# Optimization experiments

Measured on AMD Instinct MI355X. Metric: run time of the kernel, lower is better.

The kernel has to match this reference:

```python
import jax, jax.numpy as jnp
from jax import lax
import numpy as np

B, S, H = 8, 512, 768


def setup_inputs() -> dict:
    key = jax.random.key(0)
    ks = jax.random.split(key, 8)
    outputs = jax.random.normal(ks[0], (B, S, H), dtype=jnp.float32)
    starts = jax.random.randint(ks[1], (B,), S // 4, 3 * S // 4)
    mask = jnp.stack([starts, jnp.full((B,), S, dtype=starts.dtype)], axis=1)  # [B,2]
    sc = 1.0 / np.sqrt(H)
    Wa_w = jax.random.normal(ks[2], (H, H), dtype=jnp.float32) * sc
    Wa_b = jax.random.normal(ks[3], (H,), dtype=jnp.float32) * sc
    Ua_w = jax.random.normal(ks[4], (H, H), dtype=jnp.float32) * sc
    Ua_b = jax.random.normal(ks[5], (H,), dtype=jnp.float32) * sc
    Va_w = jax.random.normal(ks[6], (1, H), dtype=jnp.float32) * sc
    Va_b = jax.random.normal(ks[7], (1,), dtype=jnp.float32) * sc
    return {"outputs": outputs, "mask": mask, "Wa_w": Wa_w, "Wa_b": Wa_b,
            "Ua_w": Ua_w, "Ua_b": Ua_b, "Va_w": Va_w, "Va_b": Va_b}


def reference(outputs, mask, Wa_w, Wa_b, Ua_w, Ua_b, Va_w, Va_b):
    # outputs: [B,S,H]; mask[:,0] = start (source = tokens [0:start], summary = [start:S])
    b, s, h = outputs.shape
    Wq = jnp.einsum('bsh,oh->bso', outputs, Wa_w) + Wa_b  # query proj, [B,S,H]
    Uk = jnp.einsum('bsh,oh->bso', outputs, Ua_w) + Ua_b  # key proj,   [B,S,H]
    va = Va_w[0]  # [H]
    vb = Va_b[0]

    # Stream over query token positions to avoid a [B,S,S,H] tanh intermediate.
    def step(_, wq_t):  # wq_t: [B,H]
        m = jnp.tanh(wq_t[:, None, :] + Uk)          # [B,S,H]
        sc_t = jnp.einsum('bkh,h->bk', m, va) + vb   # [B,S]
        return None, sc_t

    _, scores = lax.scan(step, None, jnp.swapaxes(Wq, 0, 1))  # [S(query token), B, S(key)]
    scores = jnp.swapaxes(scores, 0, 1)  # [B, S_token, S_key]

    start = mask[:, 0]                              # [B]
    j = jnp.arange(s)
    # summary query j corresponds to token index start + j
    t_idx = jnp.clip(start[:, None] + j[None, :], 0, s - 1)            # [B,S]
    sc = jnp.take_along_axis(scores, t_idx[:, :, None], axis=1)       # [B,S,S]
    key_mask = (j[None, :] < start[:, None])                           # [B,S] valid source keys
    q_mask = (j[None, :] < (s - start)[:, None])                       # [B,S] valid summary queries

    sc = jnp.where(key_mask[:, None, :], sc, -1e30)
    w = jax.nn.softmax(sc, axis=-1)
    # zero out exactly where the torch code leaves zeros
    attentions = w * key_mask[:, None, :].astype(w.dtype) * q_mask[:, :, None].astype(w.dtype)
    contexts = jnp.einsum('bjk,bkh->bjh', attentions, outputs)
    return attentions, contexts
```

## Files before the change

kernel.cpp:

```cpp
#include <hip/hip_runtime.h>

typedef float  f32x4   __attribute__((ext_vector_type(4)));
typedef short  short8  __attribute__((ext_vector_type(8)));
typedef unsigned short ushort8 __attribute__((ext_vector_type(8)));

constexpr int kB = 8;
constexpr int kS = 512;
constexpr int kH = 768;
constexpr int kJM = 384;

constexpr float kTanhScale = 2.8853900817779268f;

__device__ __forceinline__ float native_exp2(float x) {
    float r; asm("v_exp_f32 %0, %1" : "=v"(r) : "v"(x)); return r;
}

__device__ __forceinline__ float waveMax(float v) {
#pragma unroll
    for (int off = 32; off > 0; off >>= 1) v = fmaxf(v, __shfl_xor(v, off, 64));
    return v;
}
__device__ __forceinline__ float waveSum(float v) {
#pragma unroll
    for (int off = 32; off > 0; off >>= 1) v += __shfl_xor(v, off, 64);
    return v;
}

__global__ __launch_bounds__(256) void k0_convert(
    const float* __restrict__ X, const float* __restrict__ Wa, const float* __restrict__ Ua,
    unsigned short* __restrict__ Xhi, unsigned short* __restrict__ Xlo,
    unsigned short* __restrict__ Wahi, unsigned short* __restrict__ Walo,
    unsigned short* __restrict__ Uahi, unsigned short* __restrict__ Ualo)
{
    const int i4 = blockIdx.x * 256 + threadIdx.x;
    const float* src; unsigned short *hi, *lo; int off;
    if (i4 < 786432)      { src = X;  hi = Xhi;  lo = Xlo;  off = i4; }
    else if (i4 < 933888) { src = Wa; hi = Wahi; lo = Walo; off = i4 - 786432; }
    else                  { src = Ua; hi = Uahi; lo = Ualo; off = i4 - 933888; }

    float4 v = *(const float4*)(src + (size_t)off * 4);
    unsigned short h[4], l[4];
#pragma unroll
    for (int c = 0; c < 4; ++c) {
        float x = (&v.x)[c];
        unsigned u = __float_as_uint(x);
        h[c] = (unsigned short)(u >> 16);
        float hf = __uint_as_float(u & 0xFFFF0000u);
        l[c] = (unsigned short)(__float_as_uint(x - hf) >> 16);
    }
    *(ushort4*)(hi + (size_t)off * 4) = make_ushort4(h[0], h[1], h[2], h[3]);
    *(ushort4*)(lo + (size_t)off * 4) = make_ushort4(l[0], l[1], l[2], l[3]);
}

__global__ __launch_bounds__(256) void k1_mfma(
    const unsigned short* __restrict__ Xhi, const unsigned short* __restrict__ Xlo,
    const unsigned short* __restrict__ W0hi, const unsigned short* __restrict__ W0lo,
    const unsigned short* __restrict__ W1hi, const unsigned short* __restrict__ W1lo,
    const float* __restrict__ b0, const float* __restrict__ b1,
    const int* __restrict__ mask,
    float* __restrict__ Eqc, float* __restrict__ EkTc)
{
    __shared__ char smem[49664];
    unsigned short* Ahi = (unsigned short*)smem;
    unsigned short* Alo = (unsigned short*)(smem + 10240);
    unsigned short* Bhi = (unsigned short*)(smem + 20480);
    unsigned short* Blo = (unsigned short*)(smem + 28160);

    const int z = blockIdx.z;
    const unsigned short* Whi = z ? W1hi : W0hi;
    const unsigned short* Wlo = z ? W1lo : W0lo;
    const float* bias = z ? b1 : b0;

    const int m0 = blockIdx.y * 128;
    const int n0 = blockIdx.x * 96;
    const int t  = threadIdx.x;
    const int bI = m0 >> 9;
    const int lb = m0 & (kS - 1);
    const int start = mask[2 * bI];

    if (z == 0) { if (lb + 128 <= start) return; }
    else        { if (lb >= start) return; }

    const int ar = t >> 1, ko = (t & 1) << 4;
    const bool doB = (ar < 96);
    const size_t aoff = (size_t)(m0 + ar) * kH + ko;
    const size_t woff = (size_t)(n0 + ar) * kH + ko;

    const int wid = t >> 6, lane = t & 63;
    const int wr = wid >> 1, wc = wid & 1;
    const int lr = lane & 15, lk = (lane >> 4) << 3;

    f32x4 acc[4][3];
#pragma unroll
    for (int mi = 0; mi < 4; ++mi)
#pragma unroll
        for (int ni = 0; ni < 3; ++ni)
#pragma unroll
            for (int r = 0; r < 4; ++r) acc[mi][ni][r] = 0.0f;

    for (int h0 = 0; h0 < kH; h0 += 32) {
        ushort8 ah0 = *(const ushort8*)(Xhi + aoff + h0);
        ushort8 ah1 = *(const ushort8*)(Xhi + aoff + h0 + 8);
        ushort8 al0 = *(const ushort8*)(Xlo + aoff + h0);
        ushort8 al1 = *(const ushort8*)(Xlo + aoff + h0 + 8);
        ushort8 bh0, bh1, bl0, bl1;
        if (doB) {
            bh0 = *(const ushort8*)(Whi + woff + h0);
            bh1 = *(const ushort8*)(Whi + woff + h0 + 8);
            bl0 = *(const ushort8*)(Wlo + woff + h0);
            bl1 = *(const ushort8*)(Wlo + woff + h0 + 8);
        }
        __syncthreads();
        *(ushort8*)(Ahi + ar * 40 + ko)     = ah0;
        *(ushort8*)(Ahi + ar * 40 + ko + 8) = ah1;
        *(ushort8*)(Alo + ar * 40 + ko)     = al0;
        *(ushort8*)(Alo + ar * 40 + ko + 8) = al1;
        if (doB) {
            *(ushort8*)(Bhi + ar * 40 + ko)     = bh0;
            *(ushort8*)(Bhi + ar * 40 + ko + 8) = bh1;
            *(ushort8*)(Blo + ar * 40 + ko)     = bl0;
            *(ushort8*)(Blo + ar * 40 + ko + 8) = bl1;
        }
        __syncthreads();

        short8 ah[4], al_[4], bh[3], bl[3];
#pragma unroll
        for (int mi = 0; mi < 4; ++mi) {
            const int row = wr * 64 + mi * 16 + lr;
            ah[mi]  = *(const short8*)(Ahi + row * 40 + lk);
            al_[mi] = *(const short8*)(Alo + row * 40 + lk);
        }
#pragma unroll
        for (int ni = 0; ni < 3; ++ni) {
            const int row = wc * 48 + ni * 16 + lr;
            bh[ni] = *(const short8*)(Bhi + row * 40 + lk);
            bl[ni] = *(const short8*)(Blo + row * 40 + lk);
        }
#pragma unroll
        for (int mi = 0; mi < 4; ++mi)
#pragma unroll
            for (int ni = 0; ni < 3; ++ni)
                acc[mi][ni] = __builtin_amdgcn_mfma_f32_16x16x32_bf16(ah[mi], bh[ni], acc[mi][ni], 0, 0, 0);
#pragma unroll
        for (int mi = 0; mi < 4; ++mi)
#pragma unroll
            for (int ni = 0; ni < 3; ++ni)
                acc[mi][ni] = __builtin_amdgcn_mfma_f32_16x16x32_bf16(al_[mi], bh[ni], acc[mi][ni], 0, 0, 0);
#pragma unroll
        for (int mi = 0; mi < 4; ++mi)
#pragma unroll
            for (int ni = 0; ni < 3; ++ni)
                acc[mi][ni] = __builtin_amdgcn_mfma_f32_16x16x32_bf16(ah[mi], bl[ni], acc[mi][ni], 0, 0, 0);
    }

    if (z == 0) {
#pragma unroll
        for (int mi = 0; mi < 4; ++mi)
#pragma unroll
            for (int ni = 0; ni < 3; ++ni) {
                const int ml = lb + wr * 64 + mi * 16 + ((lane >> 4) << 2);
                const int ng = n0 + wc * 48 + ni * 16 + lr;
                const float bn = bias[ng];
#pragma unroll
                for (int r = 0; r < 4; ++r) {
                    const int jj = ml + r - start;
                    if (jj >= 0)
                        Eqc[((size_t)bI * kJM + jj) * kH + ng] =
                            native_exp2((acc[mi][ni][r] + bn) * kTanhScale);
                }
            }
    } else {
        __syncthreads();
        float* stg = (float*)smem;
#pragma unroll
        for (int mi = 0; mi < 4; ++mi)
#pragma unroll
            for (int ni = 0; ni < 3; ++ni) {
                const int ml = wr * 64 + mi * 16 + ((lane >> 4) << 2);
                const int nl = wc * 48 + ni * 16 + lr;
                const float bn = bias[n0 + nl];
#pragma unroll
                for (int r = 0; r < 4; ++r)
                    stg[(ml + r) * 97 + nl] = native_exp2((acc[mi][ni][r] + bn) * kTanhScale);
            }
        __syncthreads();
        const int s4 = (t & 31) << 2, hb_ = t >> 5;
        const int sg = lb + s4;
#pragma unroll
        for (int u = 0; u < 12; ++u) {
            const int h = (u << 3) + hb_;
            float o[4] = { stg[(s4 + 0) * 97 + h], stg[(s4 + 1) * 97 + h],
                           stg[(s4 + 2) * 97 + h], stg[(s4 + 3) * 97 + h] };
            float* dst = EkTc + ((size_t)bI * kH + n0 + h) * kJM + sg;
            if (sg + 3 < start) {
                *(float4*)dst = make_float4(o[0], o[1], o[2], o[3]);
            } else {
#pragma unroll
                for (int e2 = 0; e2 < 4; ++e2)
                    if (sg + e2 < start) dst[e2] = o[e2];
            }
        }
    }
}

__global__ void k2a_worklist(const int* __restrict__ mask, int* __restrict__ wl)
{
    __shared__ int ne[kB], off[kB];
    const int tid = threadIdx.x;
    if (tid < kB) {
        int start = mask[2 * tid];
        ne[tid] = ((kS - start + 1) >> 1) * ((start + 63) >> 6) * 2;
    }
    __syncthreads();
    if (tid == 0) {
        int s = 0;
        for (int b = 0; b < kB; ++b) { off[b] = s; s += ne[b]; }
        wl[0] = s;
    }
    __syncthreads();
    for (int b = 0; b < kB; ++b) {
        int start = mask[2 * b];
        int nkw = (start + 63) >> 6;
        int n = ne[b], base = off[b];
        for (int t = tid; t < n; t += blockDim.x) {
            int c = t & 1, p = t >> 1;
            int jt = p / nkw, kt = p - jt * nkw;
            wl[1 + base + t] = (b << 16) | (jt << 8) | (kt << 1) | c;
        }
    }
}

__global__ __launch_bounds__(256) void k2_scores(
    const float* __restrict__ Eqc, const float* __restrict__ EkTc,
    const float* __restrict__ va, const int* __restrict__ mask,
    const int* __restrict__ wl, float* __restrict__ part0, float* __restrict__ part1)
{
    const int ntiles = wl[0];
    const int lane = threadIdx.x & 63;
    const int wslot = (blockIdx.x << 2) | (threadIdx.x >> 6);
    const int nslots = gridDim.x << 2;

    for (int w = wslot; w < ntiles; w += nslots) {
        const int e = __builtin_amdgcn_readfirstlane(wl[1 + w]);
        const int b = e >> 16, jt = (e >> 8) & 255, ktc = e & 255;
        const int kt = ktc >> 1, c = ktc & 1;
        const int start = __builtin_amdgcn_readfirstlane(mask[2 * b]);
        const int jmax = kS - start;
        const int j0 = jt << 1, k0 = kt << 6;
        const int hbase = c * 384;

        const float* eq0 = Eqc + ((size_t)b * kJM + j0) * kH + hbase;
        const float* eq1 = eq0 + kH;
        const float* ekp = EkTc + ((size_t)b * kH + hbase) * kJM + k0 + lane;
        const float* vap = va + hbase;

        float a0 = 0.0f, a1 = 0.0f;
        float eA[8], eB[8];
#pragma unroll
        for (int c2 = 0; c2 < 8; ++c2) eA[c2] = ekp[(size_t)c2 * kJM];
#pragma unroll
        for (int c2 = 0; c2 < 8; ++c2) eB[c2] = ekp[(size_t)(8 + c2) * kJM];

        for (int h0 = 0; h0 < 384; h0 += 16) {
            const bool more = (h0 + 16) < 384;
            float nA[8], nB[8];
            if (more) {
#pragma unroll
                for (int c2 = 0; c2 < 8; ++c2) nA[c2] = ekp[(size_t)(h0 + 16 + c2) * kJM];
            }
#pragma unroll
            for (int c2 = 0; c2 < 8; ++c2) {
                const float vc = vap[h0 + c2];
                float r0 = __builtin_amdgcn_rcpf(fmaf(eq0[h0 + c2], eA[c2], 1.0f));
                float r1 = __builtin_amdgcn_rcpf(fmaf(eq1[h0 + c2], eA[c2], 1.0f));
                a0 = fmaf(vc, r0, a0);
                a1 = fmaf(vc, r1, a1);
            }
            if (more) {
#pragma unroll
                for (int c2 = 0; c2 < 8; ++c2) nB[c2] = ekp[(size_t)(h0 + 24 + c2) * kJM];
#pragma unroll
                for (int c2 = 0; c2 < 8; ++c2) {
                    const float vc = vap[h0 + 8 + c2];
                    float r0 = __builtin_amdgcn_rcpf(fmaf(eq0[h0 + 8 + c2], eB[c2], 1.0f));
                    float r1 = __builtin_amdgcn_rcpf(fmaf(eq1[h0 + 8 + c2], eB[c2], 1.0f));
                    a0 = fmaf(vc, r0, a0);
                    a1 = fmaf(vc, r1, a1);
                }
#pragma unroll
                for (int c2 = 0; c2 < 8; ++c2) { eA[c2] = nA[c2]; eB[c2] = nB[c2]; }
            } else {
#pragma unroll
                for (int c2 = 0; c2 < 8; ++c2) {
                    const float vc = vap[h0 + 8 + c2];
                    float r0 = __builtin_amdgcn_rcpf(fmaf(eq0[h0 + 8 + c2], eB[c2], 1.0f));
                    float r1 = __builtin_amdgcn_rcpf(fmaf(eq1[h0 + 8 + c2], eB[c2], 1.0f));
                    a0 = fmaf(vc, r0, a0);
                    a1 = fmaf(vc, r1, a1);
                }
            }
        }

        float* srow = (c ? part1 : part0) + ((size_t)b * kS + j0) * kS + k0 + lane;
        if (j0 < jmax)     srow[0]  = -2.0f * a0;
        if (j0 + 1 < jmax) srow[kS] = -2.0f * a1;
    }
}

__global__ __launch_bounds__(256) void k3_softmax(
    float* __restrict__ attn, const float* __restrict__ part1,
    const int* __restrict__ mask)
{
    const int bx = blockIdx.x;
    const int b = bx >> 9;
    const int j = bx & (kS - 1);
    const int start = mask[2 * b];
    float* row = attn + ((size_t)b * kS + j) * kS;
    const int tid = threadIdx.x;

    if (j >= kS - start) {
        row[tid] = 0.0f;
        row[tid + 256] = 0.0f;
        return;
    }

    const float* p1row = part1 + ((size_t)b * kS + j) * kS;
    float v0 = (tid < start) ? row[tid] + p1row[tid] : -1e30f;
    float v1 = (tid + 256 < start) ? row[tid + 256] + p1row[tid + 256] : -1e30f;

    __shared__ float red[4];
    const int wid = tid >> 6;

    float m = waveMax(fmaxf(v0, v1));
    if ((tid & 63) == 0) red[wid] = m;
    __syncthreads();
    m = fmaxf(fmaxf(red[0], red[1]), fmaxf(red[2], red[3]));
    __syncthreads();

    float e0 = (tid < start) ? __expf(v0 - m) : 0.0f;
    float e1 = (tid + 256 < start) ? __expf(v1 - m) : 0.0f;
    float s = waveSum(e0 + e1);
    if ((tid & 63) == 0) red[wid] = s;
    __syncthreads();
    s = red[0] + red[1] + red[2] + red[3];

    float inv = __builtin_amdgcn_rcpf(s);
    row[tid] = e0 * inv;
    row[tid + 256] = e1 * inv;
}

__global__ __launch_bounds__(256) void k4_context(
    const float* __restrict__ attn, const float* __restrict__ outs,
    const int* __restrict__ mask, float* __restrict__ ctx)
{
    const int b = blockIdx.z;
    const int start = mask[2 * b];
    const int kmax = (start + 15) & ~15;
    const int m0 = blockIdx.y * 64;
    const int n0 = blockIdx.x * 64;

    __shared__ float As[16][68];
    __shared__ float Bs[16][68];

    const int tid = threadIdx.x;
    const int lrow = tid >> 2;
    const int lk4  = (tid & 3) << 2;
    const int brow = tid >> 4;
    const int bh4  = (tid & 15) << 2;
    const int is = tid >> 4;
    const int js = tid & 15;

    const float* arow = attn + ((size_t)b * kS + m0 + lrow) * kS + lk4;
    const float* bbase = outs + (size_t)b * kS * kH + n0 + bh4;

    float acc[4][4] = {};

    for (int k0 = 0; k0 < kmax; k0 += 16) {
        float4 av = *(const float4*)(arow + k0);
        float4 bv = *(const float4*)(bbase + (size_t)(k0 + brow) * kH);
        __syncthreads();
        As[lk4 + 0][lrow] = av.x;
        As[lk4 + 1][lrow] = av.y;
        As[lk4 + 2][lrow] = av.z;
        As[lk4 + 3][lrow] = av.w;
        *(float4*)&Bs[brow][bh4] = bv;
        __syncthreads();
#pragma unroll
        for (int kk = 0; kk < 16; ++kk) {
            const float* ap = &As[kk][is << 2];
            const float* bp = &Bs[kk][js << 2];
            float aa[4], bb[4];
#pragma unroll
            for (int c = 0; c < 4; ++c) { aa[c] = ap[c]; bb[c] = bp[c]; }
#pragma unroll
            for (int i = 0; i < 4; ++i)
#pragma unroll
                for (int j = 0; j < 4; ++j)
                    acc[i][j] = fmaf(aa[i], bb[j], acc[i][j]);
        }
    }

#pragma unroll
    for (int i = 0; i < 4; ++i) {
        int row = m0 + (is << 2) + i;
        float4 o = {acc[i][0], acc[i][1], acc[i][2], acc[i][3]};
        *(float4*)(ctx + ((size_t)b * kS + row) * kH + n0 + (js << 2)) = o;
    }
}

extern "C" void kernel_launch(void* const* d_in, const int* in_sizes, int n_in,
                              void* d_out, int out_size, void* d_ws, size_t ws_size,
                              hipStream_t stream)
{
    const float* outputs = (const float*)d_in[0];
    const int*   mask    = (const int*)d_in[1];
    const float* Wa_w    = (const float*)d_in[2];
    const float* Wa_b    = (const float*)d_in[3];
    const float* Ua_w    = (const float*)d_in[4];
    const float* Ua_b    = (const float*)d_in[5];
    const float* Va_w    = (const float*)d_in[6];

    float* attn = (float*)d_out;
    float* ctx  = attn + (size_t)kB * kS * kS;

    unsigned short* Xhi  = (unsigned short*)ctx;
    unsigned short* Xlo  = Xhi + (size_t)kB * kS * kH;
    unsigned short* Wahi = (unsigned short*)attn;
    unsigned short* Walo = Wahi + (size_t)kH * kH;
    unsigned short* Uahi = Walo + (size_t)kH * kH;
    unsigned short* Ualo = Uahi + (size_t)kH * kH;
    float* part1 = ctx;

    int* wl = (int*)d_ws;
    float* Eqc  = (float*)((char*)d_ws + 131072);
    float* EkTc = Eqc + (size_t)kB * kJM * kH;

    k0_convert<<<dim3(4224), 256, 0, stream>>>(
        outputs, Wa_w, Ua_w, Xhi, Xlo, Wahi, Walo, Uahi, Ualo);

    k1_mfma<<<dim3(kH / 96, (kB * kS) / 128, 2), 256, 0, stream>>>(
        Xhi, Xlo, Wahi, Walo, Uahi, Ualo, Wa_b, Ua_b, mask, Eqc, EkTc);

    k2a_worklist<<<dim3(1), 256, 0, stream>>>(mask, wl);
    k2_scores<<<dim3(2048), 256, 0, stream>>>(Eqc, EkTc, Va_w, mask, wl, attn, part1);

    k3_softmax<<<dim3(kB * kS), 256, 0, stream>>>(attn, part1, mask);

    k4_context<<<dim3(kH / 64, kS / 64, kB), 256, 0, stream>>>(attn, outputs, mask, ctx);
}
```

Baseline: 152.0 us.

## Drop weight low-part MFMA pass and widen score tiles to four query rows

The projection GEMM now splits only the activations into hi/lo bf16 (with round-to-nearest) and keeps a single bf16 copy of the weights. This removes one of the three MFMA passes and the weight low-part loads and LDS traffic. The score kernel now computes four query rows per wave instead of two, so each loaded key exponential is reused more often, and the grid is halved to match. The cost is lower precision in the projections and higher register pressure per wave in the score kernel.

```diff
diff --git a/kernel.cpp b/kernel.cpp
--- a/kernel.cpp
+++ b/kernel.cpp
@@ -15,6 +15,12 @@
     float r; asm("v_exp_f32 %0, %1" : "=v"(r) : "v"(x)); return r;
 }
 
+__device__ __forceinline__ unsigned short bf16_rtn(float x) {
+    unsigned u = __float_as_uint(x);
+    unsigned r = u + 0x7FFFu + ((u >> 16) & 1u);
+    return (unsigned short)(r >> 16);
+}
+
 __device__ __forceinline__ float waveMax(float v) {
 #pragma unroll
     for (int off = 32; off > 0; off >>= 1) v = fmaxf(v, __shfl_xor(v, off, 64));
@@ -29,33 +35,34 @@
 __global__ __launch_bounds__(256) void k0_convert(
     const float* __restrict__ X, const float* __restrict__ Wa, const float* __restrict__ Ua,
     unsigned short* __restrict__ Xhi, unsigned short* __restrict__ Xlo,
-    unsigned short* __restrict__ Wahi, unsigned short* __restrict__ Walo,
-    unsigned short* __restrict__ Uahi, unsigned short* __restrict__ Ualo)
+    unsigned short* __restrict__ Wahi, unsigned short* __restrict__ Uahi)
 {
     const int i4 = blockIdx.x * 256 + threadIdx.x;
-    const float* src; unsigned short *hi, *lo; int off;
-    if (i4 < 786432)      { src = X;  hi = Xhi;  lo = Xlo;  off = i4; }
-    else if (i4 < 933888) { src = Wa; hi = Wahi; lo = Walo; off = i4 - 786432; }
-    else                  { src = Ua; hi = Uahi; lo = Ualo; off = i4 - 933888; }
-
-    float4 v = *(const float4*)(src + (size_t)off * 4);
-    unsigned short h[4], l[4];
-#pragma unroll
-    for (int c = 0; c < 4; ++c) {
-        float x = (&v.x)[c];
-        unsigned u = __float_as_uint(x);
-        h[c] = (unsigned short)(u >> 16);
-        float hf = __uint_as_float(u & 0xFFFF0000u);
-        l[c] = (unsigned short)(__float_as_uint(x - hf) >> 16);
-    }
-    *(ushort4*)(hi + (size_t)off * 4) = make_ushort4(h[0], h[1], h[2], h[3]);
-    *(ushort4*)(lo + (size_t)off * 4) = make_ushort4(l[0], l[1], l[2], l[3]);
+    if (i4 < 786432) {
+        float4 v = *(const float4*)(X + (size_t)i4 * 4);
+        unsigned short h[4], l[4];
+#pragma unroll
+        for (int c = 0; c < 4; ++c) {
+            float x = (&v.x)[c];
+            h[c] = bf16_rtn(x);
+            float hf = __uint_as_float((unsigned)h[c] << 16);
+            l[c] = bf16_rtn(x - hf);
+        }
+        *(ushort4*)(Xhi + (size_t)i4 * 4) = make_ushort4(h[0], h[1], h[2], h[3]);
+        *(ushort4*)(Xlo + (size_t)i4 * 4) = make_ushort4(l[0], l[1], l[2], l[3]);
+    } else {
+        const float* src; unsigned short* hi; int off;
+        if (i4 < 933888) { src = Wa; hi = Wahi; off = i4 - 786432; }
+        else             { src = Ua; hi = Uahi; off = i4 - 933888; }
+        float4 v = *(const float4*)(src + (size_t)off * 4);
+        *(ushort4*)(hi + (size_t)off * 4) =
+            make_ushort4(bf16_rtn(v.x), bf16_rtn(v.y), bf16_rtn(v.z), bf16_rtn(v.w));
+    }
 }
 
 __global__ __launch_bounds__(256) void k1_mfma(
     const unsigned short* __restrict__ Xhi, const unsigned short* __restrict__ Xlo,
-    const unsigned short* __restrict__ W0hi, const unsigned short* __restrict__ W0lo,
-    const unsigned short* __restrict__ W1hi, const unsigned short* __restrict__ W1lo,
+    const unsigned short* __restrict__ W0hi, const unsigned short* __restrict__ W1hi,
     const float* __restrict__ b0, const float* __restrict__ b1,
     const int* __restrict__ mask,
     float* __restrict__ Eqc, float* __restrict__ EkTc)
@@ -64,11 +71,9 @@
     unsigned short* Ahi = (unsigned short*)smem;
     unsigned short* Alo = (unsigned short*)(smem + 10240);
     unsigned short* Bhi = (unsigned short*)(smem + 20480);
-    unsigned short* Blo = (unsigned short*)(smem + 28160);
 
     const int z = blockIdx.z;
     const unsigned short* Whi = z ? W1hi : W0hi;
-    const unsigned short* Wlo = z ? W1lo : W0lo;
     const float* bias = z ? b1 : b0;
 
     const int m0 = blockIdx.y * 128;
@@ -103,12 +108,10 @@
         ushort8 ah1 = *(const ushort8*)(Xhi + aoff + h0 + 8);
         ushort8 al0 = *(const ushort8*)(Xlo + aoff + h0);
         ushort8 al1 = *(const ushort8*)(Xlo + aoff + h0 + 8);
-        ushort8 bh0, bh1, bl0, bl1;
+        ushort8 bh0, bh1;
         if (doB) {
             bh0 = *(const ushort8*)(Whi + woff + h0);
             bh1 = *(const ushort8*)(Whi + woff + h0 + 8);
-            bl0 = *(const ushort8*)(Wlo + woff + h0);
-            bl1 = *(const ushort8*)(Wlo + woff + h0 + 8);
         }
         __syncthreads();
         *(ushort8*)(Ahi + ar * 40 + ko)     = ah0;
@@ -118,12 +121,10 @@
         if (doB) {
             *(ushort8*)(Bhi + ar * 40 + ko)     = bh0;
             *(ushort8*)(Bhi + ar * 40 + ko + 8) = bh1;
-            *(ushort8*)(Blo + ar * 40 + ko)     = bl0;
-            *(ushort8*)(Blo + ar * 40 + ko + 8) = bl1;
-        }
-        __syncthreads();
-
-        short8 ah[4], al_[4], bh[3], bl[3];
+        }
+        __syncthreads();
+
+        short8 ah[4], al_[4], bh[3];
 #pragma unroll
         for (int mi = 0; mi < 4; ++mi) {
             const int row = wr * 64 + mi * 16 + lr;
@@ -134,7 +135,6 @@
         for (int ni = 0; ni < 3; ++ni) {
             const int row = wc * 48 + ni * 16 + lr;
             bh[ni] = *(const short8*)(Bhi + row * 40 + lk);
-            bl[ni] = *(const short8*)(Blo + row * 40 + lk);
         }
 #pragma unroll
         for (int mi = 0; mi < 4; ++mi)
@@ -146,11 +146,6 @@
 #pragma unroll
             for (int ni = 0; ni < 3; ++ni)
                 acc[mi][ni] = __builtin_amdgcn_mfma_f32_16x16x32_bf16(al_[mi], bh[ni], acc[mi][ni], 0, 0, 0);
-#pragma unroll
-        for (int mi = 0; mi < 4; ++mi)
-#pragma unroll
-            for (int ni = 0; ni < 3; ++ni)
-                acc[mi][ni] = __builtin_amdgcn_mfma_f32_16x16x32_bf16(ah[mi], bl[ni], acc[mi][ni], 0, 0, 0);
     }
 
     if (z == 0) {
@@ -209,7 +204,7 @@
     const int tid = threadIdx.x;
     if (tid < kB) {
         int start = mask[2 * tid];
-        ne[tid] = ((kS - start + 1) >> 1) * ((start + 63) >> 6) * 2;
+        ne[tid] = ((kS - start + 3) >> 2) * ((start + 63) >> 6) * 2;
     }
     __syncthreads();
     if (tid == 0) {
@@ -221,10 +216,12 @@
     for (int b = 0; b < kB; ++b) {
         int start = mask[2 * b];
         int nkw = (start + 63) >> 6;
+        int nkc = nkw * 2;
         int n = ne[b], base = off[b];
         for (int t = tid; t < n; t += blockDim.x) {
-            int c = t & 1, p = t >> 1;
-            int jt = p / nkw, kt = p - jt * nkw;
+            int jt = t / nkc;
+            int r = t - jt * nkc;
+            int kt = r >> 1, c = r & 1;
             wl[1 + base + t] = (b << 16) | (jt << 8) | (kt << 1) | c;
         }
     }
@@ -235,6 +232,7 @@
     const float* __restrict__ va, const int* __restrict__ mask,
     const int* __restrict__ wl, float* __restrict__ part0, float* __restrict__ part1)
 {
+    constexpr int JT = 4;
     const int ntiles = wl[0];
     const int lane = threadIdx.x & 63;
     const int wslot = (blockIdx.x << 2) | (threadIdx.x >> 6);
@@ -246,15 +244,17 @@
         const int kt = ktc >> 1, c = ktc & 1;
         const int start = __builtin_amdgcn_readfirstlane(mask[2 * b]);
         const int jmax = kS - start;
-        const int j0 = jt << 1, k0 = kt << 6;
+        const int j0 = jt * JT, k0 = kt << 6;
         const int hbase = c * 384;
 
-        const float* eq0 = Eqc + ((size_t)b * kJM + j0) * kH + hbase;
-        const float* eq1 = eq0 + kH;
+        const float* eqr[JT];
+#pragma unroll
+        for (int j = 0; j < JT; ++j)
+            eqr[j] = Eqc + ((size_t)b * kJM + j0 + j) * kH + hbase;
         const float* ekp = EkTc + ((size_t)b * kH + hbase) * kJM + k0 + lane;
         const float* vap = va + hbase;
 
-        float a0 = 0.0f, a1 = 0.0f;
+        float acc[JT] = {};
         float eA[8], eB[8];
 #pragma unroll
         for (int c2 = 0; c2 < 8; ++c2) eA[c2] = ekp[(size_t)c2 * kJM];
@@ -271,39 +271,35 @@
 #pragma unroll
             for (int c2 = 0; c2 < 8; ++c2) {
                 const float vc = vap[h0 + c2];
-                float r0 = __builtin_amdgcn_rcpf(fmaf(eq0[h0 + c2], eA[c2], 1.0f));
-                float r1 = __builtin_amdgcn_rcpf(fmaf(eq1[h0 + c2], eA[c2], 1.0f));
-                a0 = fmaf(vc, r0, a0);
-                a1 = fmaf(vc, r1, a1);
+#pragma unroll
+                for (int j = 0; j < JT; ++j) {
+                    float r = __builtin_amdgcn_rcpf(fmaf(eqr[j][h0 + c2], eA[c2], 1.0f));
+                    acc[j] = fmaf(vc, r, acc[j]);
+                }
             }
             if (more) {
 #pragma unroll
                 for (int c2 = 0; c2 < 8; ++c2) nB[c2] = ekp[(size_t)(h0 + 24 + c2) * kJM];
-#pragma unroll
-                for (int c2 = 0; c2 < 8; ++c2) {
-                    const float vc = vap[h0 + 8 + c2];
-                    float r0 = __builtin_amdgcn_rcpf(fmaf(eq0[h0 + 8 + c2], eB[c2], 1.0f));
-                    float r1 = __builtin_amdgcn_rcpf(fmaf(eq1[h0 + 8 + c2], eB[c2], 1.0f));
-                    a0 = fmaf(vc, r0, a0);
-                    a1 = fmaf(vc, r1, a1);
+            }
+#pragma unroll
+            for (int c2 = 0; c2 < 8; ++c2) {
+                const float vc = vap[h0 + 8 + c2];
+#pragma unroll
+                for (int j = 0; j < JT; ++j) {
+                    float r = __builtin_amdgcn_rcpf(fmaf(eqr[j][h0 + 8 + c2], eB[c2], 1.0f));
+                    acc[j] = fmaf(vc, r, acc[j]);
                 }
+            }
+            if (more) {
 #pragma unroll
                 for (int c2 = 0; c2 < 8; ++c2) { eA[c2] = nA[c2]; eB[c2] = nB[c2]; }
-            } else {
-#pragma unroll
-                for (int c2 = 0; c2 < 8; ++c2) {
-                    const float vc = vap[h0 + 8 + c2];
-                    float r0 = __builtin_amdgcn_rcpf(fmaf(eq0[h0 + 8 + c2], eB[c2], 1.0f));
-                    float r1 = __builtin_amdgcn_rcpf(fmaf(eq1[h0 + 8 + c2], eB[c2], 1.0f));
-                    a0 = fmaf(vc, r0, a0);
-                    a1 = fmaf(vc, r1, a1);
-                }
             }
         }
 
         float* srow = (c ? part1 : part0) + ((size_t)b * kS + j0) * kS + k0 + lane;
-        if (j0 < jmax)     srow[0]  = -2.0f * a0;
-        if (j0 + 1 < jmax) srow[kS] = -2.0f * a1;
+#pragma unroll
+        for (int j = 0; j < JT; ++j)
+            if (j0 + j < jmax) srow[(size_t)j * kS] = -2.0f * acc[j];
     }
 }
 
@@ -426,9 +422,7 @@
     unsigned short* Xhi  = (unsigned short*)ctx;
     unsigned short* Xlo  = Xhi + (size_t)kB * kS * kH;
     unsigned short* Wahi = (unsigned short*)attn;
-    unsigned short* Walo = Wahi + (size_t)kH * kH;
-    unsigned short* Uahi = Walo + (size_t)kH * kH;
-    unsigned short* Ualo = Uahi + (size_t)kH * kH;
+    unsigned short* Uahi = Wahi + (size_t)kH * kH;
     float* part1 = ctx;
 
     int* wl = (int*)d_ws;
@@ -436,13 +430,13 @@
     float* EkTc = Eqc + (size_t)kB * kJM * kH;
 
     k0_convert<<<dim3(4224), 256, 0, stream>>>(
-        outputs, Wa_w, Ua_w, Xhi, Xlo, Wahi, Walo, Uahi, Ualo);
+        outputs, Wa_w, Ua_w, Xhi, Xlo, Wahi, Uahi);
 
     k1_mfma<<<dim3(kH / 96, (kB * kS) / 128, 2), 256, 0, stream>>>(
-        Xhi, Xlo, Wahi, Walo, Uahi, Ualo, Wa_b, Ua_b, mask, Eqc, EkTc);
+        Xhi, Xlo, Wahi, Uahi, Wa_b, Ua_b, mask, Eqc, EkTc);
 
     k2a_worklist<<<dim3(1), 256, 0, stream>>>(mask, wl);
-    k2_scores<<<dim3(2048), 256, 0, stream>>>(Eqc, EkTc, Va_w, mask, wl, attn, part1);
+    k2_scores<<<dim3(1024), 256, 0, stream>>>(Eqc, EkTc, Va_w, mask, wl, attn, part1);
 
     k3_softmax<<<dim3(kB * kS), 256, 0, stream>>>(attn, part1, mask);
 
```

New measurement: 145.2 us. 1.05x faster.
